# Kernel optimization log

Hardware: AMD Instinct MI355X
Metric: run time of the kernel (lower is better)

## Reference

```python
import jax, jax.numpy as jnp
import numpy as np

# Dims (match init_kwargs / input_specs)
N, N_REP, K, D = 8, 2048, 16, 3
C_IN, C_LIFT = 64, 64
C_MID = C_IN + C_LIFT   # 128
C_OUT = 128             # groups=C_OUT -> depthwise since C_MID == C_OUT
EPS = 1e-5


def setup_inputs() -> dict:
    key = jax.random.key(0)
    ks = jax.random.split(key, 10)
    w = lambda i, shape, fan_in: (jax.random.uniform(ks[i], shape, dtype=jnp.float32) * 2.0 - 1.0) / np.float32(np.sqrt(fan_in))
    return dict(
        p=jax.random.normal(ks[0], (N, N_REP, D), dtype=jnp.float32),
        P=jax.random.normal(ks[1], (N, N_REP, K, D), dtype=jnp.float32),
        F=jax.random.normal(ks[2], (N, N_REP, K, C_IN), dtype=jnp.float32),
        # BatchNorm over the D spatial channels (training-mode stats)
        bn_gamma=jnp.ones((D,), dtype=jnp.float32),
        bn_beta=jnp.zeros((D,), dtype=jnp.float32),
        # mlp_lift: Dense(D->C_LIFT) + Dense(C_LIFT->C_LIFT), ELU each
        lift_w1=w(3, (D, C_LIFT), D), lift_b1=jnp.zeros((C_LIFT,), dtype=jnp.float32),
        lift_w2=w(4, (C_LIFT, C_LIFT), C_LIFT), lift_b2=jnp.zeros((C_LIFT,), dtype=jnp.float32),
        # mid_conv: 1x1 Conv2d(D -> K) channels-last == Linear on last dim
        mid_w=w(5, (D, K), D), mid_b=jnp.zeros((K,), dtype=jnp.float32),
        # mlp: Dense(K->K) with ELU
        mlp_w=w(6, (K, K), K), mlp_b=jnp.zeros((K,), dtype=jnp.float32),
        # end_conv: Conv2d(C_MID -> C_OUT, kernel (K,1), groups=C_OUT) == depthwise
        # reduction over the neighbor dim; weight per (out_channel, neighbor)
        end_w=w(7, (C_OUT, K), K), end_b=jnp.zeros((C_OUT,), dtype=jnp.float32),
    )


def reference(p, P, F, bn_gamma, bn_beta, lift_w1, lift_b1, lift_w2, lift_b2,
              mid_w, mid_b, mlp_w, mlp_b, end_w, end_b):
    # Center neighborhoods on the representative point
    P_local = P - p[:, :, None, :]                              # (N,R,K,D)
    # Channels-last BatchNorm over D, batch stats over (N,R,K)
    mean = jnp.mean(P_local, axis=(0, 1, 2), keepdims=True)
    var = jnp.var(P_local, axis=(0, 1, 2), keepdims=True)
    P_norm = (P_local - mean) * jax.lax.rsqrt(var + EPS) * bn_gamma + bn_beta
    # Lift spatial coords to C_LIFT features (MLP of Dense+ELU layers)
    F_lift = jax.nn.elu(P_norm @ lift_w1 + lift_b1)
    F_lift = jax.nn.elu(F_lift @ lift_w2 + lift_b2)             # (N,R,K,C_LIFT)
    F_cat = jnp.concatenate([F_lift, F], axis=-1)               # (N,R,K,C_MID)
    # X-transform: 1x1 conv D->K then Dense(K->K)+ELU -> (N,R,K,K)
    X = P_norm @ mid_w + mid_b
    X = jax.nn.elu(X @ mlp_w + mlp_b)
    # Weighted aggregation: small batched matmul over the neighbor dim
    F_X = jnp.einsum('nrkj,nrjc->nrkc', X, F_cat)               # (N,R,K,C_MID)
    # Depthwise end conv: per-channel weighted sum over neighbors
    F_p = jnp.einsum('nrkc,ck->nrc', F_X, end_w) + end_b        # (N,R,C_OUT)
    return F_p
```

## Files before the change

kernel.cpp:

```cpp
#include <hip/hip_runtime.h>
#include <cstddef>

#define N_TOT   8
#define R_TOT   2048
#define NR_TOT  (N_TOT*R_TOT)
#define KK      16
#define CL      64
#define CM      128
#define EPSV    1e-5f
#define CNTF    262144.0f

typedef float    f32x4  __attribute__((ext_vector_type(4)));
typedef short    bf16x8 __attribute__((ext_vector_type(8)));
typedef unsigned u32x2  __attribute__((ext_vector_type(2)));
typedef unsigned u32x4  __attribute__((ext_vector_type(4)));

union FragU { bf16x8 f; unsigned u[4]; };

__device__ __forceinline__ float elu_f(float x){
    return x > 0.f ? x : (__expf(x) - 1.f);
}

#if defined(__has_builtin) && __has_builtin(__builtin_amdgcn_cvt_pk_bf16_f32)
__device__ __forceinline__ unsigned pk_bf16(float a, float b){
    auto v = __builtin_amdgcn_cvt_pk_bf16_f32(a, b);
    unsigned u; __builtin_memcpy(&u, &v, 4);
    return u;
}
#else
__device__ __forceinline__ unsigned pk_bf16(float a, float b){
    unsigned ua = __float_as_uint(a), ub = __float_as_uint(b);
    ua += 0x7fff + ((ua >> 16) & 1);
    ub += 0x7fff + ((ub >> 16) & 1);
    return (ua >> 16) | (ub & 0xffff0000u);
}
#endif
__device__ __forceinline__ float bf_lo(unsigned u){ return __uint_as_float(u << 16); }
__device__ __forceinline__ float bf_hi(unsigned u){ return __uint_as_float(u & 0xffff0000u); }

__device__ __forceinline__ void split4(const float* x, unsigned* o){
    unsigned h01 = pk_bf16(x[0], x[1]);
    unsigned h23 = pk_bf16(x[2], x[3]);
    float l0 = x[0] - bf_lo(h01), l1 = x[1] - bf_hi(h01);
    float l2 = x[2] - bf_lo(h23), l3 = x[3] - bf_hi(h23);
    o[0] = h01; o[1] = h23; o[2] = pk_bf16(l0, l1); o[3] = pk_bf16(l2, l3);
}

__global__ __launch_bounds__(256) void xconv_stats(
    const float* __restrict__ p, const float* __restrict__ P, float* __restrict__ ws)
{
    const int g = blockIdx.x*256 + threadIdx.x;
    const float4* P4 = (const float4*)(P + (size_t)g*12);
    float4 a = P4[0], b = P4[1], c = P4[2];
    const int nr = g >> 2;
    float pp0 = p[nr*3], pp1 = p[nr*3+1], pp2 = p[nr*3+2];
    float vx0=a.x-pp0, vx1=a.w-pp0, vx2=b.z-pp0, vx3=c.y-pp0;
    float vy0=a.y-pp1, vy1=b.x-pp1, vy2=b.w-pp1, vy3=c.z-pp1;
    float vz0=a.z-pp2, vz1=b.y-pp2, vz2=c.x-pp2, vz3=c.w-pp2;
    float s1[3], s2[3];
    s1[0]=vx0+vx1+vx2+vx3; s2[0]=vx0*vx0+vx1*vx1+vx2*vx2+vx3*vx3;
    s1[1]=vy0+vy1+vy2+vy3; s2[1]=vy0*vy0+vy1*vy1+vy2*vy2+vy3*vy3;
    s1[2]=vz0+vz1+vz2+vz3; s2[2]=vz0*vz0+vz1*vz1+vz2*vz2+vz3*vz3;

    #pragma unroll
    for (int off = 32; off > 0; off >>= 1){
        #pragma unroll
        for (int d = 0; d < 3; d++){
            s1[d] += __shfl_down(s1[d], off, 64);
            s2[d] += __shfl_down(s2[d], off, 64);
        }
    }
    __shared__ float red[4][6];
    int wave = threadIdx.x >> 6, lane = threadIdx.x & 63;
    if (lane == 0){
        #pragma unroll
        for (int d = 0; d < 3; d++){ red[wave][d] = s1[d]; red[wave][3+d] = s2[d]; }
    }
    __syncthreads();
    if (threadIdx.x < 6){
        float v = red[0][threadIdx.x] + red[1][threadIdx.x]
                + red[2][threadIdx.x] + red[3][threadIdx.x];
        atomicAdd(&ws[threadIdx.x], v);
    }
}

__global__ __launch_bounds__(256) void xconv_main(
    const float* __restrict__ p,   const float* __restrict__ P,
    const float* __restrict__ F,
    const float* __restrict__ gamma,const float* __restrict__ beta,
    const float* __restrict__ w1,  const float* __restrict__ b1,
    const float* __restrict__ w2,  const float* __restrict__ b2,
    const float* __restrict__ midw,const float* __restrict__ midb,
    const float* __restrict__ mlpw,const float* __restrict__ mlpb,
    const float* __restrict__ endw,const float* __restrict__ endb,
    const float* __restrict__ ws,  float* __restrict__ out)
{
    __shared__ float    sEndw[128*20];
    __shared__ unsigned sW1[2*64*20];
    __shared__ unsigned sW2[8*64*4];

    const int tid  = threadIdx.x;
    const int lane = tid & 63;
    const int lo16 = lane & 15;
    const int quad = lane >> 4;
    const int wave = tid >> 6;

    if (wave == 0){
        #pragma unroll
        for (int s = 0; s < 2; s++)
            #pragma unroll
            for (int j = 0; j < 8; j++){
                int q = s*32 + quad*8 + j;
                u32x2 v;
                v.x = pk_bf16(w1[q],       w1[64 + q]);
                v.y = pk_bf16(w1[128 + q], b1[q]);
                *(u32x2*)&sW1[(s*64 + lane)*20 + j*2] = v;
            }
    } else if (wave == 1){
        #pragma unroll
        for (int b = 0; b < 4; b++)
            #pragma unroll
            for (int s = 0; s < 2; s++){
                u32x4 f;
                #pragma unroll
                for (int d = 0; d < 4; d++){
                    int q0 = s*32 + quad*8 + d*2;
                    int idx = q0*64 + b*16 + lo16;
                    f[d] = pk_bf16(w2[idx], w2[idx + 64]);
                }
                *(u32x4*)&sW2[((b*2 + s)*64 + lane)*4] = f;
            }
    } else {
        int c = tid - 128;
        const float4* ep = (const float4*)endw;
        #pragma unroll
        for (int i = 0; i < 4; i++)
            *(float4*)&sEndw[c*20 + i*4] = ep[c*4 + i];
    }

    float sc[3], sh[3];
    #pragma unroll
    for (int d = 0; d < 3; d++){
        float mean = ws[d] / CNTF;
        float var  = ws[3+d] / CNTF - mean*mean;
        float s    = gamma[d] * rsqrtf(var + EPSV);
        sc[d] = s; sh[d] = beta[d] - mean*s;
    }
    FragU mlpA[2];
    {
        float mw[4];
        #pragma unroll
        for (int r = 0; r < 4; r++) mw[r] = mlpw[(quad*4 + r)*16 + lo16];
        unsigned o[4]; split4(mw, o);
        mlpA[0].u[0]=o[0]; mlpA[0].u[1]=o[1]; mlpA[0].u[2]=o[0]; mlpA[0].u[3]=o[1];
        mlpA[1].u[0]=o[2]; mlpA[1].u[1]=o[3]; mlpA[1].u[2]=o[2]; mlpA[1].u[3]=o[3];
    }
    float mlpbr[4];
    #pragma unroll
    for (int r = 0; r < 4; r++) mlpbr[r] = mlpb[quad*4 + r];
    float mw0[4], mw1[4], mw2[4], mbv[4];
    #pragma unroll
    for (int j = 0; j < 4; j++){
        int m2 = quad*4 + j;
        mw0[j] = midw[m2]; mw1[j] = midw[16 + m2]; mw2[j] = midw[32 + m2];
        mbv[j] = midb[m2];
    }
    float b2r[4];
    #pragma unroll
    for (int b = 0; b < 4; b++) b2r[b] = b2[b*16 + lo16];
    const float endb0 = endb[lane], endb1 = endb[64 + lane];

    __syncthreads();

    const int wglobal = blockIdx.x*4 + wave;

    #pragma unroll 1
    for (int it = 0; it < 4; it++){
        const int nr = wglobal*4 + it;

        float fv[4][4];
        #pragma unroll
        for (int bt = 0; bt < 4; bt++)
            #pragma unroll
            for (int r = 0; r < 4; r++)
                fv[bt][r] = F[(size_t)nr*1024 + (quad*4 + r)*64 + bt*16 + lo16];
        const int pb = nr*48 + lo16*3;
        float P0 = P[pb], P1 = P[pb+1], P2 = P[pb+2];
        float pp0 = p[nr*3], pp1 = p[nr*3+1], pp2 = p[nr*3+2];

        const float pn0 = (P0 - pp0)*sc[0] + sh[0];
        const float pn1 = (P1 - pp1)*sc[1] + sh[1];
        const float pn2 = (P2 - pp2)*sc[2] + sh[2];

        FragU hf[2];
        #pragma unroll
        for (int s = 0; s < 2; s++){
            const u32x4* wp = (const u32x4*)&sW1[(s*64 + lane)*20];
            #pragma unroll
            for (int d = 0; d < 4; d++){
                u32x4 w = wp[d];
                float h0 = bf_hi(w.y);
                h0 = fmaf(pn0, bf_lo(w.x), h0);
                h0 = fmaf(pn1, bf_hi(w.x), h0);
                h0 = fmaf(pn2, bf_lo(w.y), h0);
                float h1v = bf_hi(w.w);
                h1v = fmaf(pn0, bf_lo(w.z), h1v);
                h1v = fmaf(pn1, bf_hi(w.z), h1v);
                h1v = fmaf(pn2, bf_lo(w.w), h1v);
                hf[s].u[d] = pk_bf16(elu_f(h0), elu_f(h1v));
            }
        }

        float x0[4];
        #pragma unroll
        for (int j = 0; j < 4; j++)
            x0[j] = fmaf(pn2, mw2[j], fmaf(pn1, mw1[j], fmaf(pn0, mw0[j], mbv[j])));
        FragU x0f; split4(x0, x0f.u);

        f32x4 dx = {0.f,0.f,0.f,0.f};
        dx = __builtin_amdgcn_mfma_f32_16x16x32_bf16(mlpA[0].f, x0f.f, dx, 0,0,0);
        dx = __builtin_amdgcn_mfma_f32_16x16x32_bf16(mlpA[1].f, x0f.f, dx, 0,0,0);
        float xv[4];
        #pragma unroll
        for (int r = 0; r < 4; r++) xv[r] = elu_f(dx[r] + mlpbr[r]);
        FragU xA; split4(xv, xA.u);

        float o0 = 0.f, o1 = 0.f;

        #pragma unroll
        for (int b = 0; b < 4; b++){
            FragU wf0, wf1;
            *(u32x4*)wf0.u = *(const u32x4*)&sW2[((b*2 + 0)*64 + lane)*4];
            *(u32x4*)wf1.u = *(const u32x4*)&sW2[((b*2 + 1)*64 + lane)*4];
            f32x4 dl = {0.f,0.f,0.f,0.f};
            dl = __builtin_amdgcn_mfma_f32_16x16x32_bf16(hf[0].f, wf0.f, dl, 0,0,0);
            dl = __builtin_amdgcn_mfma_f32_16x16x32_bf16(hf[1].f, wf1.f, dl, 0,0,0);
            float fl[4];
            #pragma unroll
            for (int r = 0; r < 4; r++) fl[r] = elu_f(dl[r] + b2r[b]);
            FragU bfg;
            unsigned h01 = pk_bf16(fl[0], fl[1]), h23 = pk_bf16(fl[2], fl[3]);
            bfg.u[0] = h01; bfg.u[1] = h23; bfg.u[2] = h01; bfg.u[3] = h23;
            f32x4 da = {0.f,0.f,0.f,0.f};
            da = __builtin_amdgcn_mfma_f32_16x16x32_bf16(xA.f, bfg.f, da, 0,0,0);
            const float4 ew = *(const float4*)&sEndw[(b*16 + lo16)*20 + quad*4];
            float pt = da[0]*ew.x + da[1]*ew.y + da[2]*ew.z + da[3]*ew.w;
            pt += __shfl_xor(pt, 16, 64);
            pt += __shfl_xor(pt, 32, 64);
            if (b == quad) o0 = pt;
        }
        #pragma unroll
        for (int bt = 0; bt < 4; bt++){
            FragU bfg;
            unsigned h01 = pk_bf16(fv[bt][0], fv[bt][1]);
            unsigned h23 = pk_bf16(fv[bt][2], fv[bt][3]);
            bfg.u[0] = h01; bfg.u[1] = h23; bfg.u[2] = h01; bfg.u[3] = h23;
            f32x4 da = {0.f,0.f,0.f,0.f};
            da = __builtin_amdgcn_mfma_f32_16x16x32_bf16(xA.f, bfg.f, da, 0,0,0);
            const float4 ew = *(const float4*)&sEndw[(64 + bt*16 + lo16)*20 + quad*4];
            float pt = da[0]*ew.x + da[1]*ew.y + da[2]*ew.z + da[3]*ew.w;
            pt += __shfl_xor(pt, 16, 64);
            pt += __shfl_xor(pt, 32, 64);
            if (bt == quad) o1 = pt;
        }

        out[(size_t)nr*CM + lane]      = o0 + endb0;
        out[(size_t)nr*CM + 64 + lane] = o1 + endb1;
    }
}

extern "C" void kernel_launch(void* const* d_in, const int* in_sizes, int n_in,
                              void* d_out, int out_size, void* d_ws, size_t ws_size,
                              hipStream_t stream)
{
    const float* p     = (const float*)d_in[0];
    const float* P     = (const float*)d_in[1];
    const float* F     = (const float*)d_in[2];
    const float* gamma = (const float*)d_in[3];
    const float* beta  = (const float*)d_in[4];
    const float* w1    = (const float*)d_in[5];
    const float* b1    = (const float*)d_in[6];
    const float* w2    = (const float*)d_in[7];
    const float* b2    = (const float*)d_in[8];
    const float* midw  = (const float*)d_in[9];
    const float* midb  = (const float*)d_in[10];
    const float* mlpw  = (const float*)d_in[11];
    const float* mlpb  = (const float*)d_in[12];
    const float* endw  = (const float*)d_in[13];
    const float* endb  = (const float*)d_in[14];
    float* ws  = (float*)d_ws;
    float* out = (float*)d_out;

    hipMemsetAsync(d_ws, 0, 32, stream);
    xconv_stats<<<256, 256, 0, stream>>>(p, P, ws);
    xconv_main <<<1024, 256, 0, stream>>>(p, P, F, gamma, beta, w1, b1, w2, b2,
                                          midw, midb, mlpw, mlpb, endw, endb, ws, out);
}
```

Measured before the change: 148.4 us.

## Drop memset and atomics, prepack weights in stats kernel, double main grid

Removes the hipMemsetAsync by having each stats block write its partial sums to its own workspace slot. The main kernel then reduces all 256 partials per wave instead of reading atomically accumulated totals. The stats kernel's first block also prepacks w1/b1 (fp32) and w2 (bf16 fragments) into device globals, so main-kernel blocks only copy them into LDS instead of converting per block. w1 now stays fp32 instead of bf16. The main grid doubles to 2048 blocks with 2 points per wave, and F is converted to bf16 right after loading to save registers. Costs are the redundant per-wave reduction of 256 partials and a new dependence on globals written by the earlier kernel.

```diff
diff --git a/kernel.cpp b/kernel.cpp
--- a/kernel.cpp
+++ b/kernel.cpp
@@ -3,7 +3,6 @@
 
 #define N_TOT   8
 #define R_TOT   2048
-#define NR_TOT  (N_TOT*R_TOT)
 #define KK      16
 #define CL      64
 #define CM      128
@@ -12,10 +11,12 @@
 
 typedef float    f32x4  __attribute__((ext_vector_type(4)));
 typedef short    bf16x8 __attribute__((ext_vector_type(8)));
-typedef unsigned u32x2  __attribute__((ext_vector_type(2)));
 typedef unsigned u32x4  __attribute__((ext_vector_type(4)));
 
 union FragU { bf16x8 f; unsigned u[4]; };
+
+__device__ float    g_w1f[72*4];
+__device__ unsigned g_w2p[8*64*4];
 
 __device__ __forceinline__ float elu_f(float x){
     return x > 0.f ? x : (__expf(x) - 1.f);
@@ -47,9 +48,12 @@
 }
 
 __global__ __launch_bounds__(256) void xconv_stats(
-    const float* __restrict__ p, const float* __restrict__ P, float* __restrict__ ws)
+    const float* __restrict__ p, const float* __restrict__ P,
+    const float* __restrict__ w1, const float* __restrict__ b1,
+    const float* __restrict__ w2, float* __restrict__ ws)
 {
-    const int g = blockIdx.x*256 + threadIdx.x;
+    const int tid = threadIdx.x;
+    const int g = blockIdx.x*256 + tid;
     const float4* P4 = (const float4*)(P + (size_t)g*12);
     float4 a = P4[0], b = P4[1], c = P4[2];
     const int nr = g >> 2;
@@ -71,16 +75,36 @@
         }
     }
     __shared__ float red[4][6];
-    int wave = threadIdx.x >> 6, lane = threadIdx.x & 63;
+    int wave = tid >> 6, lane = tid & 63;
     if (lane == 0){
         #pragma unroll
         for (int d = 0; d < 3; d++){ red[wave][d] = s1[d]; red[wave][3+d] = s2[d]; }
     }
     __syncthreads();
-    if (threadIdx.x < 6){
-        float v = red[0][threadIdx.x] + red[1][threadIdx.x]
-                + red[2][threadIdx.x] + red[3][threadIdx.x];
-        atomicAdd(&ws[threadIdx.x], v);
+    float v = 0.f;
+    if (tid < 6) v = red[0][tid] + red[1][tid] + red[2][tid] + red[3][tid];
+    if (tid < 8) ws[blockIdx.x*8 + tid] = v;
+
+    if (blockIdx.x == 0){
+        if (wave == 0){
+            f32x4 w4 = { w1[lane], w1[64+lane], w1[128+lane], b1[lane] };
+            *(f32x4*)&g_w1f[((lane>>3)*9 + (lane&7))*4] = w4;
+        } else if (wave == 1){
+            const int lo16 = lane & 15, quad = lane >> 4;
+            #pragma unroll
+            for (int bb = 0; bb < 4; bb++)
+                #pragma unroll
+                for (int s = 0; s < 2; s++){
+                    u32x4 f;
+                    #pragma unroll
+                    for (int d = 0; d < 4; d++){
+                        int q0 = s*32 + quad*8 + d*2;
+                        int idx = q0*64 + bb*16 + lo16;
+                        f[d] = pk_bf16(w2[idx], w2[idx + 64]);
+                    }
+                    *(u32x4*)&g_w2p[((bb*2 + s)*64 + lane)*4] = f;
+                }
+        }
     }
 }
 
@@ -88,16 +112,16 @@
     const float* __restrict__ p,   const float* __restrict__ P,
     const float* __restrict__ F,
     const float* __restrict__ gamma,const float* __restrict__ beta,
-    const float* __restrict__ w1,  const float* __restrict__ b1,
-    const float* __restrict__ w2,  const float* __restrict__ b2,
+    const float* __restrict__ mlpw,const float* __restrict__ mlpb,
     const float* __restrict__ midw,const float* __restrict__ midb,
-    const float* __restrict__ mlpw,const float* __restrict__ mlpb,
+    const float* __restrict__ b2,
     const float* __restrict__ endw,const float* __restrict__ endb,
     const float* __restrict__ ws,  float* __restrict__ out)
 {
     __shared__ float    sEndw[128*20];
-    __shared__ unsigned sW1[2*64*20];
+    __shared__ float    sW1f[72*4];
     __shared__ unsigned sW2[8*64*4];
+    __shared__ float    sMid[16*4];
 
     const int tid  = threadIdx.x;
     const int lane = tid & 63;
@@ -106,46 +130,54 @@
     const int wave = tid >> 6;
 
     if (wave == 0){
-        #pragma unroll
-        for (int s = 0; s < 2; s++)
-            #pragma unroll
-            for (int j = 0; j < 8; j++){
-                int q = s*32 + quad*8 + j;
-                u32x2 v;
-                v.x = pk_bf16(w1[q],       w1[64 + q]);
-                v.y = pk_bf16(w1[128 + q], b1[q]);
-                *(u32x2*)&sW1[(s*64 + lane)*20 + j*2] = v;
-            }
+        *(f32x4*)&sW1f[lane*4] = *(const f32x4*)&g_w1f[lane*4];
+        if (lane < 8)
+            *(f32x4*)&sW1f[(64+lane)*4] = *(const f32x4*)&g_w1f[(64+lane)*4];
     } else if (wave == 1){
         #pragma unroll
-        for (int b = 0; b < 4; b++)
-            #pragma unroll
-            for (int s = 0; s < 2; s++){
-                u32x4 f;
-                #pragma unroll
-                for (int d = 0; d < 4; d++){
-                    int q0 = s*32 + quad*8 + d*2;
-                    int idx = q0*64 + b*16 + lo16;
-                    f[d] = pk_bf16(w2[idx], w2[idx + 64]);
-                }
-                *(u32x4*)&sW2[((b*2 + s)*64 + lane)*4] = f;
-            }
+        for (int i = 0; i < 8; i++)
+            *(u32x4*)&sW2[(i*64+lane)*4] = *(const u32x4*)&g_w2p[(i*64+lane)*4];
     } else {
         int c = tid - 128;
-        const float4* ep = (const float4*)endw;
+        const f32x4* ep = (const f32x4*)endw;
         #pragma unroll
         for (int i = 0; i < 4; i++)
-            *(float4*)&sEndw[c*20 + i*4] = ep[c*4 + i];
-    }
-
+            *(f32x4*)&sEndw[c*20 + i*4] = ep[c*4 + i];
+        if (c >= 112){
+            int m2 = c - 112;
+            f32x4 mv = { midw[m2], midw[16+m2], midw[32+m2], midb[m2] };
+            *(f32x4*)&sMid[m2*4] = mv;
+        }
+    }
+
+    float s1[3] = {0.f,0.f,0.f}, s2[3] = {0.f,0.f,0.f};
+    {
+        const f32x4* wp = (const f32x4*)ws;
+        #pragma unroll
+        for (int i = 0; i < 4; i++){
+            int row = lane + i*64;
+            f32x4 pa = wp[row*2], pb = wp[row*2 + 1];
+            s1[0] += pa.x; s1[1] += pa.y; s1[2] += pa.z;
+            s2[0] += pa.w; s2[1] += pb.x; s2[2] += pb.y;
+        }
+        #pragma unroll
+        for (int off = 32; off > 0; off >>= 1){
+            #pragma unroll
+            for (int d = 0; d < 3; d++){
+                s1[d] += __shfl_xor(s1[d], off, 64);
+                s2[d] += __shfl_xor(s2[d], off, 64);
+            }
+        }
+    }
     float sc[3], sh[3];
     #pragma unroll
     for (int d = 0; d < 3; d++){
-        float mean = ws[d] / CNTF;
-        float var  = ws[3+d] / CNTF - mean*mean;
+        float mean = s1[d] * (1.0f/CNTF);
+        float var  = s2[d] * (1.0f/CNTF) - mean*mean;
         float s    = gamma[d] * rsqrtf(var + EPSV);
         sc[d] = s; sh[d] = beta[d] - mean*s;
     }
+
     FragU mlpA[2];
     {
         float mw[4];
@@ -158,13 +190,6 @@
     float mlpbr[4];
     #pragma unroll
     for (int r = 0; r < 4; r++) mlpbr[r] = mlpb[quad*4 + r];
-    float mw0[4], mw1[4], mw2[4], mbv[4];
-    #pragma unroll
-    for (int j = 0; j < 4; j++){
-        int m2 = quad*4 + j;
-        mw0[j] = midw[m2]; mw1[j] = midw[16 + m2]; mw2[j] = midw[32 + m2];
-        mbv[j] = midb[m2];
-    }
     float b2r[4];
     #pragma unroll
     for (int b = 0; b < 4; b++) b2r[b] = b2[b*16 + lo16];
@@ -175,19 +200,22 @@
     const int wglobal = blockIdx.x*4 + wave;
 
     #pragma unroll 1
-    for (int it = 0; it < 4; it++){
-        const int nr = wglobal*4 + it;
-
-        float fv[4][4];
-        #pragma unroll
-        for (int bt = 0; bt < 4; bt++)
-            #pragma unroll
-            for (int r = 0; r < 4; r++)
-                fv[bt][r] = F[(size_t)nr*1024 + (quad*4 + r)*64 + bt*16 + lo16];
+    for (int it = 0; it < 2; it++){
+        const int nr = wglobal*2 + it;
+
         const int pb = nr*48 + lo16*3;
         float P0 = P[pb], P1 = P[pb+1], P2 = P[pb+2];
         float pp0 = p[nr*3], pp1 = p[nr*3+1], pp2 = p[nr*3+2];
 
+        unsigned fh01[4], fh23[4];
+        #pragma unroll
+        for (int bt = 0; bt < 4; bt++){
+            const size_t fb = (size_t)nr*1024 + (size_t)(quad*4)*64 + bt*16 + lo16;
+            float f0 = F[fb], f1 = F[fb + 64], f2 = F[fb + 128], f3 = F[fb + 192];
+            fh01[bt] = pk_bf16(f0, f1);
+            fh23[bt] = pk_bf16(f2, f3);
+        }
+
         const float pn0 = (P0 - pp0)*sc[0] + sh[0];
         const float pn1 = (P1 - pp1)*sc[1] + sh[1];
         const float pn2 = (P2 - pp2)*sc[2] + sh[2];
@@ -195,26 +223,22 @@
         FragU hf[2];
         #pragma unroll
         for (int s = 0; s < 2; s++){
-            const u32x4* wp = (const u32x4*)&sW1[(s*64 + lane)*20];
+            const f32x4* wp = (const f32x4*)&sW1f[((s*4 + quad)*9)*4];
             #pragma unroll
             for (int d = 0; d < 4; d++){
-                u32x4 w = wp[d];
-                float h0 = bf_hi(w.y);
-                h0 = fmaf(pn0, bf_lo(w.x), h0);
-                h0 = fmaf(pn1, bf_hi(w.x), h0);
-                h0 = fmaf(pn2, bf_lo(w.y), h0);
-                float h1v = bf_hi(w.w);
-                h1v = fmaf(pn0, bf_lo(w.z), h1v);
-                h1v = fmaf(pn1, bf_hi(w.z), h1v);
-                h1v = fmaf(pn2, bf_lo(w.w), h1v);
+                f32x4 wa = wp[2*d], wb = wp[2*d+1];
+                float h0  = fmaf(pn2, wa.z, fmaf(pn1, wa.y, fmaf(pn0, wa.x, wa.w)));
+                float h1v = fmaf(pn2, wb.z, fmaf(pn1, wb.y, fmaf(pn0, wb.x, wb.w)));
                 hf[s].u[d] = pk_bf16(elu_f(h0), elu_f(h1v));
             }
         }
 
         float x0[4];
         #pragma unroll
-        for (int j = 0; j < 4; j++)
-            x0[j] = fmaf(pn2, mw2[j], fmaf(pn1, mw1[j], fmaf(pn0, mw0[j], mbv[j])));
+        for (int j = 0; j < 4; j++){
+            f32x4 mw = *(const f32x4*)&sMid[(quad*4 + j)*4];
+            x0[j] = fmaf(pn2, mw.z, fmaf(pn1, mw.y, fmaf(pn0, mw.x, mw.w)));
+        }
         FragU x0f; split4(x0, x0f.u);
 
         f32x4 dx = {0.f,0.f,0.f,0.f};
@@ -252,9 +276,8 @@
         #pragma unroll
         for (int bt = 0; bt < 4; bt++){
             FragU bfg;
-            unsigned h01 = pk_bf16(fv[bt][0], fv[bt][1]);
-            unsigned h23 = pk_bf16(fv[bt][2], fv[bt][3]);
-            bfg.u[0] = h01; bfg.u[1] = h23; bfg.u[2] = h01; bfg.u[3] = h23;
+            bfg.u[0] = fh01[bt]; bfg.u[1] = fh23[bt];
+            bfg.u[2] = fh01[bt]; bfg.u[3] = fh23[bt];
             f32x4 da = {0.f,0.f,0.f,0.f};
             da = __builtin_amdgcn_mfma_f32_16x16x32_bf16(xA.f, bfg.f, da, 0,0,0);
             const float4 ew = *(const float4*)&sEndw[(64 + bt*16 + lo16)*20 + quad*4];
@@ -291,8 +314,7 @@
     float* ws  = (float*)d_ws;
     float* out = (float*)d_out;
 
-    hipMemsetAsync(d_ws, 0, 32, stream);
-    xconv_stats<<<256, 256, 0, stream>>>(p, P, ws);
-    xconv_main <<<1024, 256, 0, stream>>>(p, P, F, gamma, beta, w1, b1, w2, b2,
-                                          midw, midb, mlpw, mlpb, endw, endb, ws, out);
-}
+    xconv_stats<<<256, 256, 0, stream>>>(p, P, w1, b1, w2, ws);
+    xconv_main <<<2048, 256, 0, stream>>>(p, P, F, gamma, beta, mlpw, mlpb,
+                                          midw, midb, b2, endw, endb, ws, out);
+}
```

New measurement: 148.7 us. No clear change (+0.3%).
